# Kernel tuning notes

Measured on AMD Instinct MI355X. Metric: run time of the kernel, lower is better.

The kernel has to match this reference:

```python
import jax, jax.numpy as jnp
import numpy as np

B, CIN, COUT, H, W, REP = 8, 512, 64, 28, 28, 1024


def setup_inputs() -> dict:
    key = jax.random.key(0)
    ks = jax.random.split(key, 7)
    scale_conv = 1.0 / np.sqrt(CIN * 9)
    scale_fc6 = 1.0 / np.sqrt(CIN * COUT)
    scale_fc7 = 1.0 / np.sqrt(REP)
    return {
        "x": jax.random.normal(ks[0], (B, CIN, H, W), jnp.float32),
        "conv_w": jax.random.normal(ks[1], (COUT, CIN, 3, 3), jnp.float32) * scale_conv,
        "conv_b": jax.random.normal(ks[2], (COUT,), jnp.float32) * scale_conv,
        "fc6_w": jax.random.normal(ks[3], (REP, CIN * COUT), jnp.float32) * scale_fc6,
        "fc6_b": jax.random.normal(ks[4], (REP,), jnp.float32) * scale_fc6,
        "fc7_w": jax.random.normal(ks[5], (REP, REP), jnp.float32) * scale_fc7,
        "fc7_b": jax.random.normal(ks[6], (REP,), jnp.float32) * scale_fc7,
    }


def reference(x, conv_w, conv_b, fc6_w, fc6_b, fc7_w, fc7_b):
    # attention_map: (B, COUT, H, W) -- 3x3 conv, stride 1, pad 1 ('SAME')
    am = jax.lax.conv_general_dilated(
        x, conv_w, window_strides=(1, 1), padding="SAME",
        dimension_numbers=("NCHW", "OIHW", "NCHW"),
    ) + conv_b[None, :, None, None]
    # outer product (B, CIN, COUT, H, W) then global max-pool over H, W
    outer = am[:, None, :, :, :] * x[:, :, None, :, :]
    x_pool = jnp.max(outer, axis=(3, 4))  # (B, CIN, COUT)
    # eval-mode path: pooled features -> fc6 -> relu -> fc7 -> relu
    flat = x_pool.reshape(x.shape[0], -1)  # (B, CIN*COUT)
    h = jax.nn.relu(flat @ fc6_w.T + fc6_b)
    out = jax.nn.relu(h @ fc7_w.T + fc7_b)
    return (out, x_pool)
```

## Files before the change

kernel.cpp:

```cpp
#include <hip/hip_runtime.h>

typedef __attribute__((ext_vector_type(4))) float f32x4;
typedef __attribute__((ext_vector_type(8))) __bf16 bf16x8;
typedef __attribute__((ext_vector_type(8))) unsigned short ushort8;

static __device__ __forceinline__ unsigned short f2bf(float f) {
  unsigned u = __float_as_uint(f);
  u += 0x7fffu + ((u >> 16) & 1u);
  return (unsigned short)(u >> 16);
}

__global__ __launch_bounds__(256, 1) void k_xpose(
    const float* __restrict__ x, const float* __restrict__ cw,
    unsigned short* __restrict__ xT, unsigned short* __restrict__ wpk) {
  int bid = blockIdx.x;
  int t = threadIdx.x;
  if (bid < 896) {
    __shared__ float xl[64 * 57];
    int pt = bid % 14, cit = (bid / 14) & 7, b = bid / 112;
    int p0 = pt * 56, ci0 = cit * 64;
#pragma unroll
    for (int i = 0; i < 4; ++i) {
      int idx = i * 256 + t;
      if (idx < 896) {
        int ci = idx / 14, p4 = (idx % 14) * 4;
        f32x4 v = *reinterpret_cast<const f32x4*>(
            x + ((size_t)(b * 512 + ci0 + ci)) * 784 + p0 + p4);
        *reinterpret_cast<f32x4*>(&xl[ci * 57 + p4]) = v;
      }
    }
    __syncthreads();
#pragma unroll
    for (int i = 0; i < 2; ++i) {
      int idx = i * 256 + t;
      if (idx < 448) {
        int p = idx >> 3, c8 = (idx & 7) * 8;
        ushort8 o;
#pragma unroll
        for (int j = 0; j < 8; ++j) o[j] = f2bf(xl[(c8 + j) * 57 + p]);
        *reinterpret_cast<ushort8*>(
            xT + ((size_t)(b * 784 + p0 + p)) * 512 + ci0 + c8) = o;
      }
    }
  } else {
    int o0 = (bid - 896) * 4096 + t * 16;
    ushort8 w0, w1;
#pragma unroll
    for (int j = 0; j < 16; ++j) {
      int o = o0 + j;
      int ci = o & 511, co = (o >> 9) & 63, tap = o >> 15;
      unsigned short v = f2bf(cw[((size_t)(co * 512 + ci)) * 9 + tap]);
      if (j < 8) w0[j] = v; else w1[j - 8] = v;
    }
    *reinterpret_cast<ushort8*>(wpk + o0) = w0;
    *reinterpret_cast<ushort8*>(wpk + o0 + 8) = w1;
  }
}

#define CPAD 56
__global__ __launch_bounds__(128, 1) void k_conv(
    const unsigned short* __restrict__ xT, const unsigned short* __restrict__ wpk,
    const float* __restrict__ cb, float* __restrict__ am_part) {
  __shared__ unsigned short wl[9 * 32 * CPAD];
  __shared__ unsigned short xl[168 * CPAD];
  int bid = blockIdx.x;
  int s  = bid & 3;
  int c2 = (bid >> 2) & 1;
  int px = (bid >> 3) % 7;
  int b  = bid / 56;
  int t = threadIdx.x;
  int W = t >> 6, lane = t & 63;
  int co_base = c2 * 32;
  int p0 = px * 112, h0 = px * 4;
  int n = lane & 15, kg = lane >> 4;

  int lrow0[7], wc[7];
#pragma unroll
  for (int f = 0; f < 7; ++f) {
    int pit = f * 16 + n;
    lrow0[f] = pit / 28 + 1;
    wc[f]    = pit % 28;
  }
  f32x4 acc[7];
  f32x4 cb4 = {0.f, 0.f, 0.f, 0.f};
  if (s == 0)
    cb4 = *reinterpret_cast<const f32x4*>(cb + co_base + W * 16 + kg * 4);
#pragma unroll
  for (int f = 0; f < 7; ++f) acc[f] = cb4;
  const ushort8 bzero = {0, 0, 0, 0, 0, 0, 0, 0};

  for (int c = 0; c < 4; ++c) {
    int ci_c = s * 128 + c * 32;
    __syncthreads();
#pragma unroll
    for (int i = 0; i < 9; ++i) {
      int q = i * 128 + t;
      int tapco = q >> 2, ci8 = (q & 3) * 8;
      int tap = tapco >> 5, co_l = tapco & 31;
      ushort8 v = *reinterpret_cast<const ushort8*>(
          wpk + ((size_t)(tap * 64 + co_base + co_l)) * 512 + ci_c + ci8);
      *reinterpret_cast<ushort8*>(&wl[(tap * 32 + co_l) * CPAD + ci8]) = v;
    }
#pragma unroll
    for (int i = 0; i < 6; ++i) {
      int q = i * 128 + t;
      if (q < 672) {
        int pos = q >> 2, ci8 = (q & 3) * 8;
        int lr = pos / 28, c_ = pos % 28;
        int h = h0 - 1 + lr;
        ushort8 v = bzero;
        if (h >= 0 && h < 28)
          v = *reinterpret_cast<const ushort8*>(
              xT + ((size_t)(b * 784 + h * 28 + c_)) * 512 + ci_c + ci8);
        *reinterpret_cast<ushort8*>(&xl[pos * CPAD + ci8]) = v;
      }
    }
    __syncthreads();
#pragma unroll
    for (int tap = 0; tap < 9; ++tap) {
      int dh = tap / 3 - 1, dw = tap % 3 - 1;
      bf16x8 a = *reinterpret_cast<const bf16x8*>(
          &wl[(tap * 32 + W * 16 + n) * CPAD + kg * 8]);
#pragma unroll
      for (int f = 0; f < 7; ++f) {
        int wcd = wc[f] + dw;
        bool valid = (unsigned)wcd < 28u;
        int pos = (lrow0[f] + dh) * 28 + wcd;
        int posc = valid ? pos : 0;
        ushort8 bv = *reinterpret_cast<const ushort8*>(&xl[posc * CPAD + kg * 8]);
        if (!valid) bv = bzero;
        acc[f] = __builtin_amdgcn_mfma_f32_16x16x32_bf16(
            a, __builtin_bit_cast(bf16x8, bv), acc[f], 0, 0, 0);
      }
    }
  }
#pragma unroll
  for (int f = 0; f < 7; ++f) {
    int p  = p0 + f * 16 + n;
    int co = co_base + W * 16 + kg * 4;
    *reinterpret_cast<f32x4*>(
        am_part + ((size_t)((s * 8 + b) * 784 + p)) * 64 + co) = acc[f];
  }
}

__global__ __launch_bounds__(256, 1) void k_pool(
    const float* __restrict__ x, const float* __restrict__ am_part,
    float* __restrict__ pmax) {
  __shared__ float aml[112 * 64];
  __shared__ float xls[112 * 65];
  int bid = blockIdx.x;
  int pc  = bid % 7;
  int cit = (bid / 7) & 7;
  int b   = bid / 56;
  int t = threadIdx.x;
  int p0 = pc * 112;
#pragma unroll
  for (int i = 0; i < 7; ++i) {
    int idx = i * 256 + t;
    int p = idx >> 4, cog = (idx & 15) * 4;
    size_t o0 = ((size_t)(b * 784 + p0 + p)) * 64 + cog;
    f32x4 v = *reinterpret_cast<const f32x4*>(am_part + o0);
#pragma unroll
    for (int s2 = 1; s2 < 4; ++s2)
      v = v + *reinterpret_cast<const f32x4*>(am_part + o0 + (size_t)s2 * 8 * 784 * 64);
    *reinterpret_cast<f32x4*>(&aml[p * 64 + cog]) = v;
  }
#pragma unroll
  for (int i = 0; i < 7; ++i) {
    int idx = i * 256 + t;
    int ci = idx / 28, p4 = (idx % 28) * 4;
    f32x4 v = *reinterpret_cast<const f32x4*>(
        x + ((size_t)(b * 512 + cit * 64 + ci)) * 784 + p0 + p4);
#pragma unroll
    for (int q = 0; q < 4; ++q) xls[(p4 + q) * 65 + ci] = v[q];
  }
  __syncthreads();
  int co4 = (t & 15) * 4, ci4 = (t >> 4) * 4;
  float m[4][4];
#pragma unroll
  for (int i = 0; i < 4; ++i)
#pragma unroll
    for (int j = 0; j < 4; ++j) m[i][j] = -3.4e38f;
  for (int p = 0; p < 112; ++p) {
    f32x4 a4 = *reinterpret_cast<const f32x4*>(&aml[p * 64 + co4]);
    f32x4 xv = *reinterpret_cast<const f32x4*>(&xls[p * 65 + ci4]);
#pragma unroll
    for (int i = 0; i < 4; ++i)
#pragma unroll
      for (int j = 0; j < 4; ++j) m[i][j] = fmaxf(m[i][j], xv[i] * a4[j]);
  }
#pragma unroll
  for (int i = 0; i < 4; ++i) {
    f32x4 v = {m[i][0], m[i][1], m[i][2], m[i][3]};
    *reinterpret_cast<f32x4*>(
        pmax + ((size_t)((pc * 8 + b) * 512 + cit * 64 + ci4 + i)) * 64 + co4) = v;
  }
}

__global__ __launch_bounds__(256, 1) void k_combine(
    const float* __restrict__ pmax, float* __restrict__ xpool) {
  size_t idx = ((size_t)blockIdx.x * 256 + threadIdx.x) * 4;
  f32x4 v = *reinterpret_cast<const f32x4*>(pmax + idx);
#pragma unroll
  for (int pc = 1; pc < 7; ++pc) {
    f32x4 u = *reinterpret_cast<const f32x4*>(pmax + (size_t)pc * 262144 + idx);
#pragma unroll
    for (int j = 0; j < 4; ++j) v[j] = fmaxf(v[j], u[j]);
  }
  *reinterpret_cast<f32x4*>(xpool + idx) = v;
}

__global__ __launch_bounds__(256, 1) void k_fc6(
    const float* __restrict__ flat, const float* __restrict__ w6,
    float* __restrict__ part6) {
  __shared__ float red[4][8][66];
  int bid = blockIdx.x;
  int kc = bid & 7, rg = bid >> 3;
  int t = threadIdx.x, W = t >> 6, lane = t & 63;
  int r0 = rg * 8;
  float acc[8][8];
#pragma unroll
  for (int r = 0; r < 8; ++r)
#pragma unroll
    for (int b = 0; b < 8; ++b) acc[r][b] = 0.f;
  int kbase = kc * 4096 + t * 4;
#pragma unroll
  for (int step = 0; step < 4; ++step) {
    int k = kbase + step * 1024;
    f32x4 f4[8], w4[8];
#pragma unroll
    for (int b = 0; b < 8; ++b)
      f4[b] = *reinterpret_cast<const f32x4*>(flat + (size_t)b * 32768 + k);
#pragma unroll
    for (int r = 0; r < 8; ++r)
      w4[r] = *reinterpret_cast<const f32x4*>(w6 + (size_t)(r0 + r) * 32768 + k);
#pragma unroll
    for (int r = 0; r < 8; ++r)
#pragma unroll
      for (int b = 0; b < 8; ++b)
        acc[r][b] += w4[r][0] * f4[b][0] + w4[r][1] * f4[b][1] +
                     w4[r][2] * f4[b][2] + w4[r][3] * f4[b][3];
  }
#pragma unroll
  for (int r = 0; r < 8; ++r)
#pragma unroll
    for (int b = 0; b < 8; ++b) {
      float v = acc[r][b];
      v += __shfl_down(v, 32, 64);
      v += __shfl_down(v, 16, 64);
      v += __shfl_down(v, 8, 64);
      acc[r][b] = v;
    }
  if (lane < 8) {
#pragma unroll
    for (int r = 0; r < 8; ++r)
#pragma unroll
      for (int b = 0; b < 8; ++b) red[W][lane][r * 8 + b] = acc[r][b];
  }
  __syncthreads();
  if (t < 64) {
    float sum = 0.f;
#pragma unroll
    for (int w = 0; w < 4; ++w)
#pragma unroll
      for (int l = 0; l < 8; ++l) sum += red[w][l][t];
    int r = t >> 3, b = t & 7;
    part6[(size_t)kc * 8192 + (r0 + r) * 8 + b] = sum;
  }
}

__global__ __launch_bounds__(256, 1) void k_h(
    const float* __restrict__ part6, const float* __restrict__ b6,
    float* __restrict__ h) {
  int idx = blockIdx.x * 256 + threadIdx.x;
  int r = idx >> 3, b = idx & 7;
  float s = b6[r];
#pragma unroll
  for (int kc = 0; kc < 8; ++kc) s += part6[(size_t)kc * 8192 + r * 8 + b];
  h[b * 1024 + r] = fmaxf(s, 0.f);
}

__global__ __launch_bounds__(256, 1) void k_fc7(
    const float* __restrict__ h, const float* __restrict__ w7,
    const float* __restrict__ b7, float* __restrict__ out) {
  int bid = blockIdx.x;
  int t = threadIdx.x, W = t >> 6, lane = t & 63;
  int r = bid * 4 + W;
  float acc[8] = {0, 0, 0, 0, 0, 0, 0, 0};
#pragma unroll
  for (int step = 0; step < 4; ++step) {
    int k = step * 256 + lane * 4;
    f32x4 w4 = *reinterpret_cast<const f32x4*>(w7 + (size_t)r * 1024 + k);
#pragma unroll
    for (int b = 0; b < 8; ++b) {
      f32x4 h4 = *reinterpret_cast<const f32x4*>(h + b * 1024 + k);
      acc[b] += w4[0] * h4[0] + w4[1] * h4[1] + w4[2] * h4[2] + w4[3] * h4[3];
    }
  }
#pragma unroll
  for (int b = 0; b < 8; ++b) {
    float v = acc[b];
#pragma unroll
    for (int off = 32; off > 0; off >>= 1) v += __shfl_down(v, off, 64);
    acc[b] = v;
  }
  if (lane == 0) {
#pragma unroll
    for (int b = 0; b < 8; ++b) out[b * 1024 + r] = fmaxf(acc[b] + b7[r], 0.f);
  }
}

extern "C" void kernel_launch(void* const* d_in, const int* in_sizes, int n_in,
                              void* d_out, int out_size, void* d_ws, size_t ws_size,
                              hipStream_t stream) {
  const float* x  = (const float*)d_in[0];
  const float* cw = (const float*)d_in[1];
  const float* cb = (const float*)d_in[2];
  const float* w6 = (const float*)d_in[3];
  const float* b6 = (const float*)d_in[4];
  const float* w7 = (const float*)d_in[5];
  const float* b7 = (const float*)d_in[6];
  float* out   = (float*)d_out;
  float* xpool = out + 8192;

  char* ws = (char*)d_ws;
  unsigned short* xT  = (unsigned short*)(ws);
  unsigned short* wpk = (unsigned short*)(ws + 6422528);
  float* am_part      = (float*)(ws + 7012352);
  float* pmax         = (float*)(ws + 13434880);
  float* part6        = (float*)(ws + 20774912);
  float* hbuf         = (float*)(ws + 21037056);

  hipLaunchKernelGGL(k_xpose,   dim3(968),  dim3(256), 0, stream, x, cw, xT, wpk);
  hipLaunchKernelGGL(k_conv,    dim3(448),  dim3(128), 0, stream, xT, wpk, cb, am_part);
  hipLaunchKernelGGL(k_pool,    dim3(448),  dim3(256), 0, stream, x, am_part, pmax);
  hipLaunchKernelGGL(k_combine, dim3(256),  dim3(256), 0, stream, pmax, xpool);
  hipLaunchKernelGGL(k_fc6,     dim3(1024), dim3(256), 0, stream, xpool, w6, part6);
  hipLaunchKernelGGL(k_h,       dim3(32),   dim3(256), 0, stream, part6, b6, hbuf);
  hipLaunchKernelGGL(k_fc7,     dim3(256),  dim3(256), 0, stream, hbuf, w7, b7, out);
}
```

Baseline: 96.19 us.

## Retile pooling on bf16 transposed input and relax fc6 launch bounds

The pooling kernel now reads the already-transposed bf16 copy of x instead of transposing fp32 x in shared memory. Each thread computes an 8x8 channel tile over half the positions, so each block covers 128 input channels and the grid drops to 224 blocks. The combine step now merges 14 partial-max slices instead of 7, and the workspace offsets move to fit the larger buffer. Separately, fc6 loads one weight vector at a time and allows up to 4 blocks per CU to raise occupancy. Using bf16 x in the max-product adds rounding error to x_pool, and the smaller pool grid leaves some CUs idle.

After: 364.1 us. 3.79x slower.

```diff
diff --git a/kernel.cpp b/kernel.cpp
--- a/kernel.cpp
+++ b/kernel.cpp
@@ -8,6 +8,9 @@
   unsigned u = __float_as_uint(f);
   u += 0x7fffu + ((u >> 16) & 1u);
   return (unsigned short)(u >> 16);
+}
+static __device__ __forceinline__ float bf2f(unsigned short s) {
+  return __uint_as_float(((unsigned)s) << 16);
 }
 
 __global__ __launch_bounds__(256, 1) void k_xpose(
@@ -143,57 +146,78 @@
   }
 }
 
+#define XPAD 144
+#define APAD 72
 __global__ __launch_bounds__(256, 1) void k_pool(
-    const float* __restrict__ x, const float* __restrict__ am_part,
+    const unsigned short* __restrict__ xT, const float* __restrict__ am_part,
     float* __restrict__ pmax) {
-  __shared__ float aml[112 * 64];
-  __shared__ float xls[112 * 65];
+  __shared__ unsigned short xls[112 * XPAD];
+  __shared__ float aml[112 * APAD];
   int bid = blockIdx.x;
   int pc  = bid % 7;
-  int cit = (bid / 7) & 7;
-  int b   = bid / 56;
+  int cit = (bid / 7) & 3;
+  int b   = bid / 28;
   int t = threadIdx.x;
-  int p0 = pc * 112;
+  int p0 = pc * 112, ci0 = cit * 128;
 #pragma unroll
   for (int i = 0; i < 7; ++i) {
     int idx = i * 256 + t;
-    int p = idx >> 4, cog = (idx & 15) * 4;
-    size_t o0 = ((size_t)(b * 784 + p0 + p)) * 64 + cog;
+    int p = idx >> 4, c8 = (idx & 15) * 8;
+    ushort8 v = *reinterpret_cast<const ushort8*>(
+        xT + ((size_t)(b * 784 + p0 + p)) * 512 + ci0 + c8);
+    *reinterpret_cast<ushort8*>(&xls[p * XPAD + c8]) = v;
+  }
+#pragma unroll
+  for (int i = 0; i < 7; ++i) {
+    int idx = i * 256 + t;
+    int p = idx >> 4, co4 = (idx & 15) * 4;
+    size_t o0 = ((size_t)(b * 784 + p0 + p)) * 64 + co4;
     f32x4 v = *reinterpret_cast<const f32x4*>(am_part + o0);
 #pragma unroll
     for (int s2 = 1; s2 < 4; ++s2)
       v = v + *reinterpret_cast<const f32x4*>(am_part + o0 + (size_t)s2 * 8 * 784 * 64);
-    *reinterpret_cast<f32x4*>(&aml[p * 64 + cog]) = v;
-  }
-#pragma unroll
-  for (int i = 0; i < 7; ++i) {
-    int idx = i * 256 + t;
-    int ci = idx / 28, p4 = (idx % 28) * 4;
-    f32x4 v = *reinterpret_cast<const f32x4*>(
-        x + ((size_t)(b * 512 + cit * 64 + ci)) * 784 + p0 + p4);
-#pragma unroll
-    for (int q = 0; q < 4; ++q) xls[(p4 + q) * 65 + ci] = v[q];
+    *reinterpret_cast<f32x4*>(&aml[p * APAD + co4]) = v;
   }
   __syncthreads();
-  int co4 = (t & 15) * 4, ci4 = (t >> 4) * 4;
-  float m[4][4];
-#pragma unroll
-  for (int i = 0; i < 4; ++i)
-#pragma unroll
-    for (int j = 0; j < 4; ++j) m[i][j] = -3.4e38f;
-  for (int p = 0; p < 112; ++p) {
-    f32x4 a4 = *reinterpret_cast<const f32x4*>(&aml[p * 64 + co4]);
-    f32x4 xv = *reinterpret_cast<const f32x4*>(&xls[p * 65 + ci4]);
-#pragma unroll
-    for (int i = 0; i < 4; ++i)
-#pragma unroll
-      for (int j = 0; j < 4; ++j) m[i][j] = fmaxf(m[i][j], xv[i] * a4[j]);
-  }
-#pragma unroll
-  for (int i = 0; i < 4; ++i) {
-    f32x4 v = {m[i][0], m[i][1], m[i][2], m[i][3]};
-    *reinterpret_cast<f32x4*>(
-        pmax + ((size_t)((pc * 8 + b) * 512 + cit * 64 + ci4 + i)) * 64 + co4) = v;
+  int half = t >> 7;
+  int t1 = t & 127;
+  int ci8 = (t1 >> 3) * 8, co8 = (t1 & 7) * 8;
+  int pb = half * 56;
+  float m[8][8];
+#pragma unroll
+  for (int i = 0; i < 8; ++i)
+#pragma unroll
+    for (int j = 0; j < 8; ++j) m[i][j] = -3.4e38f;
+  for (int pp = 0; pp < 56; pp += 2) {
+    int p = pb + pp;
+    ushort8 xs0 = *reinterpret_cast<const ushort8*>(&xls[p * XPAD + ci8]);
+    ushort8 xs1 = *reinterpret_cast<const ushort8*>(&xls[(p + 1) * XPAD + ci8]);
+    f32x4 a00 = *reinterpret_cast<const f32x4*>(&aml[p * APAD + co8]);
+    f32x4 a01 = *reinterpret_cast<const f32x4*>(&aml[p * APAD + co8 + 4]);
+    f32x4 a10 = *reinterpret_cast<const f32x4*>(&aml[(p + 1) * APAD + co8]);
+    f32x4 a11 = *reinterpret_cast<const f32x4*>(&aml[(p + 1) * APAD + co8 + 4]);
+    float xv0[8], xv1[8], av0[8], av1[8];
+#pragma unroll
+    for (int i = 0; i < 8; ++i) { xv0[i] = bf2f(xs0[i]); xv1[i] = bf2f(xs1[i]); }
+#pragma unroll
+    for (int j = 0; j < 4; ++j) {
+      av0[j] = a00[j]; av0[j + 4] = a01[j];
+      av1[j] = a10[j]; av1[j + 4] = a11[j];
+    }
+#pragma unroll
+    for (int i = 0; i < 8; ++i)
+#pragma unroll
+      for (int j = 0; j < 8; ++j)
+        m[i][j] = fmaxf(fmaxf(m[i][j], xv0[i] * av0[j]), xv1[i] * av1[j]);
+  }
+  int pcc = pc * 2 + half;
+#pragma unroll
+  for (int i = 0; i < 8; ++i) {
+    f32x4 v0 = {m[i][0], m[i][1], m[i][2], m[i][3]};
+    f32x4 v1 = {m[i][4], m[i][5], m[i][6], m[i][7]};
+    size_t o = ((size_t)((pcc * 8 + b) * 512 + ci0 + ci8 + i)) * 64 + co8;
+    *reinterpret_cast<f32x4*>(pmax + o) = v0;
+    *reinterpret_cast<f32x4*>(pmax + o + 4) = v1;
   }
 }
 
@@ -202,15 +226,15 @@
   size_t idx = ((size_t)blockIdx.x * 256 + threadIdx.x) * 4;
   f32x4 v = *reinterpret_cast<const f32x4*>(pmax + idx);
 #pragma unroll
-  for (int pc = 1; pc < 7; ++pc) {
-    f32x4 u = *reinterpret_cast<const f32x4*>(pmax + (size_t)pc * 262144 + idx);
+  for (int pcc = 1; pcc < 14; ++pcc) {
+    f32x4 u = *reinterpret_cast<const f32x4*>(pmax + (size_t)pcc * 262144 + idx);
 #pragma unroll
     for (int j = 0; j < 4; ++j) v[j] = fmaxf(v[j], u[j]);
   }
   *reinterpret_cast<f32x4*>(xpool + idx) = v;
 }
 
-__global__ __launch_bounds__(256, 1) void k_fc6(
+__global__ __launch_bounds__(256, 4) void k_fc6(
     const float* __restrict__ flat, const float* __restrict__ w6,
     float* __restrict__ part6) {
   __shared__ float red[4][8][66];
@@ -227,19 +251,18 @@
 #pragma unroll
   for (int step = 0; step < 4; ++step) {
     int k = kbase + step * 1024;
-    f32x4 f4[8], w4[8];
+    f32x4 f4[8];
 #pragma unroll
     for (int b = 0; b < 8; ++b)
       f4[b] = *reinterpret_cast<const f32x4*>(flat + (size_t)b * 32768 + k);
 #pragma unroll
-    for (int r = 0; r < 8; ++r)
-      w4[r] = *reinterpret_cast<const f32x4*>(w6 + (size_t)(r0 + r) * 32768 + k);
-#pragma unroll
-    for (int r = 0; r < 8; ++r)
+    for (int r = 0; r < 8; ++r) {
+      f32x4 w4 = *reinterpret_cast<const f32x4*>(w6 + (size_t)(r0 + r) * 32768 + k);
 #pragma unroll
       for (int b = 0; b < 8; ++b)
-        acc[r][b] += w4[r][0] * f4[b][0] + w4[r][1] * f4[b][1] +
-                     w4[r][2] * f4[b][2] + w4[r][3] * f4[b][3];
+        acc[r][b] += w4[0] * f4[b][0] + w4[1] * f4[b][1] +
+                     w4[2] * f4[b][2] + w4[3] * f4[b][3];
+    }
   }
 #pragma unroll
   for (int r = 0; r < 8; ++r)
@@ -328,12 +351,12 @@
   unsigned short* wpk = (unsigned short*)(ws + 6422528);
   float* am_part      = (float*)(ws + 7012352);
   float* pmax         = (float*)(ws + 13434880);
-  float* part6        = (float*)(ws + 20774912);
-  float* hbuf         = (float*)(ws + 21037056);
+  float* part6        = (float*)(ws + 28114944);
+  float* hbuf         = (float*)(ws + 28377088);
 
   hipLaunchKernelGGL(k_xpose,   dim3(968),  dim3(256), 0, stream, x, cw, xT, wpk);
   hipLaunchKernelGGL(k_conv,    dim3(448),  dim3(128), 0, stream, xT, wpk, cb, am_part);
-  hipLaunchKernelGGL(k_pool,    dim3(448),  dim3(256), 0, stream, x, am_part, pmax);
+  hipLaunchKernelGGL(k_pool,    dim3(224),  dim3(256), 0, stream, xT, am_part, pmax);
   hipLaunchKernelGGL(k_combine, dim3(256),  dim3(256), 0, stream, pmax, xpool);
   hipLaunchKernelGGL(k_fc6,     dim3(1024), dim3(256), 0, stream, xpool, w6, part6);
   hipLaunchKernelGGL(k_h,       dim3(32),   dim3(256), 0, stream, part6, b6, hbuf);
```
